# Kernel optimization log

Hardware: AMD Instinct MI355X
Metric: run time of the kernel (lower is better)

Reference implementation:

```python
import jax, jax.numpy as jnp
import numpy as np

NEG = float(-2**32 + 1)  # mask fill value used by the original module
H = 8  # number of heads (matches init kwarg h)


def setup_inputs() -> dict:
    key = jax.random.key(0)
    B, S, D, Q, V = 4, 2048, 512, 64, 64
    ks = jax.random.split(key, 10)
    sc = 1.0 / np.sqrt(D)
    x = jax.random.normal(ks[0], (B, S, D), jnp.float32)
    padding_mask = jax.random.randint(ks[1], (B, S), 0, 2, jnp.int32)
    Wq = jax.random.normal(ks[2], (H * Q, D), jnp.float32) * sc
    bq = jnp.zeros((H * Q,), jnp.float32)
    Wk = jax.random.normal(ks[3], (H * Q, D), jnp.float32) * sc
    bk = jnp.zeros((H * Q,), jnp.float32)
    Wv = jax.random.normal(ks[4], (H * V, D), jnp.float32) * sc
    bv = jnp.zeros((H * V,), jnp.float32)
    Wo = jax.random.normal(ks[5], (D, H * V), jnp.float32) * (1.0 / np.sqrt(H * V))
    bo = jnp.zeros((D,), jnp.float32)
    return {"x": x, "padding_mask": padding_mask, "Wq": Wq, "bq": bq,
            "Wk": Wk, "bk": bk, "Wv": Wv, "bv": bv, "Wo": Wo, "bo": bo}


def reference(x, padding_mask, Wq, bq, Wk, bk, Wv, bv, Wo, bo):
    # stage is hardcoded to 'train' (mask=True in init), so the causal branch runs.
    B, S, D = x.shape
    q_dim = Wq.shape[0] // H
    v_dim = Wv.shape[0] // H

    def split_heads(t, d):
        # torch: cat(chunk(h, dim=-1), dim=0) -> head-major [H*B, S, d]
        return t.reshape(B, S, H, d).transpose(2, 0, 1, 3).reshape(H * B, S, d)

    Qh = split_heads(x @ Wq.T + bq, q_dim)   # [H*B, S, q]
    Kh = split_heads(x @ Wk.T + bk, q_dim)
    Vh = split_heads(x @ Wv.T + bv, v_dim)

    score = jnp.einsum('nsd,ntd->nst', Qh, Kh) / jnp.sqrt(jnp.float32(q_dim))  # [H*B,S,S]
    pre_score = score  # module returns the UNMASKED scores (saved before masking)

    # causal mask (mask=True, stage=='train')
    causal = jnp.tril(jnp.ones((S, S), jnp.float32))
    score = jnp.where(causal > 0, score, NEG)

    # padding mask: built batch-major [B*H,S,S] while score is head-major [H*B,...]
    # -- faithful reproduction of the original ordering quirk.
    pm = jnp.broadcast_to(padding_mask[:, None, None, :], (B, H, S, S)).reshape(B * H, S, S)
    score = jnp.where(pm == 0, NEG, score)

    attn = jax.nn.softmax(score, axis=-1)
    out = jnp.einsum('nst,ntd->nsd', attn, Vh)  # [H*B, S, v]

    # torch: cat(chunk(h, dim=0), dim=-1) -> [B, S, H*v]
    heads = out.reshape(H, B, S, v_dim).transpose(1, 2, 0, 3).reshape(B, S, H * v_dim)
    self_attention = heads @ Wo.T + bo
    return self_attention, pre_score
```

## Files before the change

### kernel.cpp

```cpp
#include <hip/hip_runtime.h>
#include <hip/hip_fp16.h>
#include <math.h>

typedef _Float16 f16;
typedef _Float16 f16x8 __attribute__((ext_vector_type(8)));
typedef _Float16 f16x4 __attribute__((ext_vector_type(4)));
typedef float    f32x4 __attribute__((ext_vector_type(4)));

#define MFMA16(a,b,c) __builtin_amdgcn_mfma_f32_16x16x32_f16(a, b, c, 0, 0, 0)

#define MASKNEG (-6.0e9f)
#define LOG2E   1.44269504088896f

__global__ __launch_bounds__(256) void qkv_gemm(
    const float* __restrict__ x,
    const float* __restrict__ Wq, const float* __restrict__ bq,
    const float* __restrict__ Wk, const float* __restrict__ bk,
    const float* __restrict__ Wv, const float* __restrict__ bv,
    f16* __restrict__ Qws, f16* __restrict__ Kws, f16* __restrict__ Vt)
{
    __shared__ f16 Al[128 * 48];
    __shared__ f16 Wl[64 * 48];

    const int tid = threadIdx.x;
    const int bx  = blockIdx.x;
    const int m0  = blockIdx.y * 128;
    const int widx = bx >> 3;
    const int n0   = (bx & 7) * 64;

    const float* W    = (widx == 0) ? Wq : (widx == 1) ? Wk : Wv;
    const float* bias = (widx == 0) ? bq : (widx == 1) ? bk : bv;

    const int wid = tid >> 6, lane = tid & 63;
    const int g = lane >> 4, c = lane & 15;
    const int wm = (wid >> 1) * 64, wn = (wid & 1) * 32;

    const int sr = tid >> 3, sc = tid & 7;

    f32x4 acc[4][2] = {};

    for (int kk = 0; kk < 512; kk += 32) {
        __syncthreads();
        #pragma unroll
        for (int rr = 0; rr < 4; ++rr) {
            int row = sr + rr * 32;
            float4 v = *(const float4*)&x[(size_t)(m0 + row) * 512 + kk + sc * 4];
            f16x4 h4 = {(f16)v.x, (f16)v.y, (f16)v.z, (f16)v.w};
            *(f16x4*)&Al[row * 48 + sc * 4] = h4;
        }
        #pragma unroll
        for (int rr = 0; rr < 2; ++rr) {
            int row = sr + rr * 32;
            float4 v = *(const float4*)&W[(size_t)(n0 + row) * 512 + kk + sc * 4];
            f16x4 h4 = {(f16)v.x, (f16)v.y, (f16)v.z, (f16)v.w};
            *(f16x4*)&Wl[row * 48 + sc * 4] = h4;
        }
        __syncthreads();

        f16x8 b0 = *(const f16x8*)&Wl[(wn +  0 + c) * 48 + g * 8];
        f16x8 b1 = *(const f16x8*)&Wl[(wn + 16 + c) * 48 + g * 8];
        #pragma unroll
        for (int mf = 0; mf < 4; ++mf) {
            f16x8 a = *(const f16x8*)&Al[(wm + mf * 16 + c) * 48 + g * 8];
            acc[mf][0] = MFMA16(a, b0, acc[mf][0]);
            acc[mf][1] = MFMA16(a, b1, acc[mf][1]);
        }
    }

    #pragma unroll
    for (int nf = 0; nf < 2; ++nf) {
        int cc = n0 + wn + nf * 16 + c;
        float bval = bias[cc];
        #pragma unroll
        for (int mf = 0; mf < 4; ++mf) {
            if (widx < 2) {
                f16* outp = (widx == 0) ? Qws : Kws;
                #pragma unroll
                for (int r = 0; r < 4; ++r) {
                    int mrow = m0 + wm + mf * 16 + g * 4 + r;
                    outp[(size_t)mrow * 512 + cc] = (f16)(acc[mf][nf][r] + bval);
                }
            } else {
                int h  = n0 >> 6;
                int d  = wn + nf * 16 + c;
                int t0 = m0 + wm + mf * 16 + g * 4;
                int b  = t0 >> 11;
                int ts = t0 & 2047;
                int nn = h * 4 + b;
                f16x4 pk = {(f16)(acc[mf][nf][0] + bval), (f16)(acc[mf][nf][1] + bval),
                            (f16)(acc[mf][nf][2] + bval), (f16)(acc[mf][nf][3] + bval)};
                *(f16x4*)&Vt[((size_t)(nn * 64 + d)) * 2048 + ts] = pk;
            }
        }
    }
}

__global__ __launch_bounds__(256) void vsum_kernel(
    const f16* __restrict__ Vt, float* __restrict__ Vsum)
{
    const int row  = blockIdx.x * 4 + (threadIdx.x >> 6);
    const int lane = threadIdx.x & 63;
    const f16* p = Vt + (size_t)row * 2048;
    float s = 0.f;
    #pragma unroll
    for (int i = 0; i < 4; ++i) {
        f16x8 v = *(const f16x8*)&p[i * 512 + lane * 8];
        #pragma unroll
        for (int j = 0; j < 8; ++j) s += (float)v[j];
    }
    #pragma unroll
    for (int off = 1; off < 64; off <<= 1) s += __shfl_xor(s, off, 64);
    if (lane == 0) Vsum[row] = s;
}

__global__ __launch_bounds__(256) void attn_kernel(
    const f16* __restrict__ Qws, const f16* __restrict__ Kws,
    const f16* __restrict__ Vt,  const int* __restrict__ pmask,
    const float* __restrict__ Vsum,
    float* __restrict__ pre_score, f16* __restrict__ attn_out)
{
    __shared__ f16 Kl[64 * 72];
    __shared__ f16 Vl[64 * 72];
    __shared__ f16 Pl[4][32 * 72];

    const int tid = threadIdx.x;
    const int wid = tid >> 6, lane = tid & 63;
    const int g = lane >> 4, c = lane & 15;
    const int qt = blockIdx.x;
    const int n  = blockIdx.y;
    const int h = n >> 2, b = n & 3;
    const int pmrow = n >> 3;
    const int qlo = qt * 64 + wid * 16;
    const int qhi = (31 - qt) * 64 + wid * 16;

    f16x8 qf[2][2];
    #pragma unroll
    for (int ks = 0; ks < 2; ++ks) {
        qf[0][ks] = *(const f16x8*)
            &Qws[(size_t)(b * 2048 + qlo + c) * 512 + h * 64 + ks * 32 + g * 8];
        qf[1][ks] = *(const f16x8*)
            &Qws[(size_t)(b * 2048 + qhi + c) * 512 + h * 64 + ks * 32 + g * 8];
    }

    f32x4 o[2][4] = {};
    float mrow[2][4], lrow[2][4];
    #pragma unroll
    for (int mi = 0; mi < 2; ++mi)
        #pragma unroll
        for (int r = 0; r < 4; ++r) { mrow[mi][r] = -INFINITY; lrow[mi][r] = 0.0f; }

    const int sr = tid >> 3, sc = tid & 7;
    const int* pmp = pmask + pmrow * 2048;
    const f16* Kbase = Kws + (size_t)(b * 2048) * 512 + h * 64;
    const f16* Vbase = Vt + (size_t)(n * 64) * 2048;
    float* prow0 = pre_score + ((size_t)n * 2048 + qlo + g * 4) * 2048;
    float* prow1 = pre_score + ((size_t)n * 2048 + qhi + g * 4) * 2048;

    auto tile = [&](int kt, bool L0, bool L1) __attribute__((always_inline)) {
        __syncthreads();
        #pragma unroll
        for (int rr = 0; rr < 2; ++rr) {
            int row = sr + rr * 32;
            *(uint4*)&Kl[row * 72 + sc * 8] =
                *(const uint4*)&Kbase[(size_t)(kt * 64 + row) * 512 + sc * 8];
            *(uint4*)&Vl[row * 72 + sc * 8] =
                *(const uint4*)&Vbase[(size_t)row * 2048 + kt * 64 + sc * 8];
        }
        __syncthreads();

        f32x4 s[2][4] = {};
        #pragma unroll
        for (int nf = 0; nf < 4; ++nf)
            #pragma unroll
            for (int ks = 0; ks < 2; ++ks) {
                f16x8 kf = *(const f16x8*)&Kl[(nf * 16 + c) * 72 + ks * 32 + g * 8];
                s[0][nf] = MFMA16(qf[0][ks], kf, s[0][nf]);
                s[1][nf] = MFMA16(qf[1][ks], kf, s[1][nf]);
            }

        #pragma unroll
        for (int nf = 0; nf < 4; ++nf) {
            int tg  = kt * 64 + nf * 16 + c;
            int pmv = pmp[tg];
            #pragma unroll
            for (int r = 0; r < 4; ++r) {
                float v0 = s[0][nf][r] * 0.125f;
                float v1 = s[1][nf][r] * 0.125f;
                __builtin_nontemporal_store(v0, &prow0[(size_t)r * 2048 + tg]);
                __builtin_nontemporal_store(v1, &prow1[(size_t)r * 2048 + tg]);
                if (L0) s[0][nf][r] = (tg <= qlo + g * 4 + r && pmv != 0)
                                    ? v0 * LOG2E : MASKNEG;
                if (L1) s[1][nf][r] = (tg <= qhi + g * 4 + r && pmv != 0)
                                    ? v1 * LOG2E : MASKNEG;
            }
        }

        #pragma unroll
        for (int mi = 0; mi < 2; ++mi) {
            if (mi == 0 && !L0) continue;
            if (mi == 1 && !L1) continue;
            float alpha[4];
            #pragma unroll
            for (int r = 0; r < 4; ++r) {
                float rm = fmaxf(fmaxf(s[mi][0][r], s[mi][1][r]),
                                 fmaxf(s[mi][2][r], s[mi][3][r]));
                rm = fmaxf(rm, __shfl_xor(rm, 1, 64));
                rm = fmaxf(rm, __shfl_xor(rm, 2, 64));
                rm = fmaxf(rm, __shfl_xor(rm, 4, 64));
                rm = fmaxf(rm, __shfl_xor(rm, 8, 64));
                float mn = fmaxf(mrow[mi][r], rm);
                alpha[r] = exp2f(mrow[mi][r] - mn);
                mrow[mi][r] = mn;
            }
            float rs[4] = {0.f, 0.f, 0.f, 0.f};
            #pragma unroll
            for (int nf = 0; nf < 4; ++nf)
                #pragma unroll
                for (int r = 0; r < 4; ++r) {
                    float p = exp2f(s[mi][nf][r] - mrow[mi][r]);
                    rs[r] += p;
                    Pl[wid][(mi * 16 + g * 4 + r) * 72 + nf * 16 + c] = (f16)p;
                }
            #pragma unroll
            for (int r = 0; r < 4; ++r) {
                float t = rs[r];
                t += __shfl_xor(t, 1, 64);
                t += __shfl_xor(t, 2, 64);
                t += __shfl_xor(t, 4, 64);
                t += __shfl_xor(t, 8, 64);
                lrow[mi][r] = lrow[mi][r] * alpha[r] + t;
                #pragma unroll
                for (int dn = 0; dn < 4; ++dn) o[mi][dn][r] *= alpha[r];
            }
        }
        asm volatile("s_waitcnt lgkmcnt(0)" ::: "memory");

        #pragma unroll
        for (int ks = 0; ks < 2; ++ks) {
            f16x8 pa0, pa1;
            if (L0) pa0 = *(const f16x8*)&Pl[wid][( 0 + c) * 72 + ks * 32 + g * 8];
            if (L1) pa1 = *(const f16x8*)&Pl[wid][(16 + c) * 72 + ks * 32 + g * 8];
            #pragma unroll
            for (int dn = 0; dn < 4; ++dn) {
                f16x8 vb = *(const f16x8*)&Vl[(dn * 16 + c) * 72 + ks * 32 + g * 8];
                if (L0) o[0][dn] = MFMA16(pa0, vb, o[0][dn]);
                if (L1) o[1][dn] = MFMA16(pa1, vb, o[1][dn]);
            }
        }
    };

    for (int kt = 0; kt <= qt; ++kt)          tile(kt, true,  true);
    for (int kt = qt + 1; kt <= 31 - qt; ++kt) tile(kt, false, true);

    for (int kt = 32 - qt; kt < 32; ++kt) {
        f32x4 s[2][4] = {};
        #pragma unroll
        for (int nf = 0; nf < 4; ++nf)
            #pragma unroll
            for (int ks = 0; ks < 2; ++ks) {
                f16x8 kf = *(const f16x8*)
                    &Kbase[(size_t)(kt * 64 + nf * 16 + c) * 512 + ks * 32 + g * 8];
                s[0][nf] = MFMA16(qf[0][ks], kf, s[0][nf]);
                s[1][nf] = MFMA16(qf[1][ks], kf, s[1][nf]);
            }
        #pragma unroll
        for (int nf = 0; nf < 4; ++nf) {
            int tg = kt * 64 + nf * 16 + c;
            #pragma unroll
            for (int r = 0; r < 4; ++r) {
                __builtin_nontemporal_store(s[0][nf][r] * 0.125f,
                                            &prow0[(size_t)r * 2048 + tg]);
                __builtin_nontemporal_store(s[1][nf][r] * 0.125f,
                                            &prow1[(size_t)r * 2048 + tg]);
            }
        }
    }

    #pragma unroll
    for (int mi = 0; mi < 2; ++mi) {
        int qb = mi ? qhi : qlo;
        #pragma unroll
        for (int r = 0; r < 4; ++r) {
            int srow = qb + g * 4 + r;
            bool dead = (mrow[mi][r] == MASKNEG);
            float inv_l = dead ? 0.f : 1.0f / lrow[mi][r];
            #pragma unroll
            for (int dn = 0; dn < 4; ++dn) {
                float val = dead ? Vsum[n * 64 + dn * 16 + c] * (1.0f / 2048.0f)
                                 : o[mi][dn][r] * inv_l;
                attn_out[(size_t)(b * 2048 + srow) * 512 + h * 64 + dn * 16 + c] = (f16)val;
            }
        }
    }
}

__global__ __launch_bounds__(256) void out_gemm(
    const f16* __restrict__ Aattn, const float* __restrict__ Wo,
    const float* __restrict__ bo, float* __restrict__ outp)
{
    __shared__ f16 Al[128 * 48];
    __shared__ f16 Wl[64 * 48];

    const int tid = threadIdx.x;
    const int n0 = blockIdx.x * 64;
    const int m0 = blockIdx.y * 128;
    const int wid = tid >> 6, lane = tid & 63;
    const int g = lane >> 4, c = lane & 15;
    const int wm = (wid >> 1) * 64, wn = (wid & 1) * 32;

    const int sr4 = tid >> 2, sc4 = tid & 3;
    const int sr8 = tid >> 3, sc8 = tid & 7;

    f32x4 acc[4][2] = {};

    for (int kk = 0; kk < 512; kk += 32) {
        __syncthreads();
        #pragma unroll
        for (int rr = 0; rr < 2; ++rr) {
            int row = sr4 + rr * 64;
            *(uint4*)&Al[row * 48 + sc4 * 8] =
                *(const uint4*)&Aattn[(size_t)(m0 + row) * 512 + kk + sc4 * 8];
        }
        #pragma unroll
        for (int rr = 0; rr < 2; ++rr) {
            int row = sr8 + rr * 32;
            float4 v = *(const float4*)&Wo[(size_t)(n0 + row) * 512 + kk + sc8 * 4];
            f16x4 h4 = {(f16)v.x, (f16)v.y, (f16)v.z, (f16)v.w};
            *(f16x4*)&Wl[row * 48 + sc8 * 4] = h4;
        }
        __syncthreads();

        f16x8 b0 = *(const f16x8*)&Wl[(wn +  0 + c) * 48 + g * 8];
        f16x8 b1 = *(const f16x8*)&Wl[(wn + 16 + c) * 48 + g * 8];
        #pragma unroll
        for (int mf = 0; mf < 4; ++mf) {
            f16x8 a = *(const f16x8*)&Al[(wm + mf * 16 + c) * 48 + g * 8];
            acc[mf][0] = MFMA16(a, b0, acc[mf][0]);
            acc[mf][1] = MFMA16(a, b1, acc[mf][1]);
        }
    }

    #pragma unroll
    for (int nf = 0; nf < 2; ++nf) {
        int cc = n0 + wn + nf * 16 + c;
        float bval = bo[cc];
        #pragma unroll
        for (int mf = 0; mf < 4; ++mf)
            #pragma unroll
            for (int r = 0; r < 4; ++r)
                outp[(size_t)(m0 + wm + mf * 16 + g * 4 + r) * 512 + cc] =
                    acc[mf][nf][r] + bval;
    }
}

extern "C" void kernel_launch(void* const* d_in, const int* in_sizes, int n_in,
                              void* d_out, int out_size, void* d_ws, size_t ws_size,
                              hipStream_t stream)
{
    (void)in_sizes; (void)n_in; (void)out_size; (void)ws_size;

    const float* x  = (const float*)d_in[0];
    const int*   pm = (const int*)  d_in[1];
    const float* Wq = (const float*)d_in[2];
    const float* bq = (const float*)d_in[3];
    const float* Wk = (const float*)d_in[4];
    const float* bk = (const float*)d_in[5];
    const float* Wv = (const float*)d_in[6];
    const float* bv = (const float*)d_in[7];
    const float* Wo = (const float*)d_in[8];
    const float* bo = (const float*)d_in[9];

    float* out = (float*)d_out;
    float* pre = out + (size_t)4 * 2048 * 512;

    f16*   Qws  = (f16*)d_ws;
    f16*   Kws  = Qws + (size_t)8192 * 512;
    f16*   Vt   = Kws + (size_t)8192 * 512;
    f16*   Aat  = Vt  + (size_t)2048 * 2048;
    float* Vsum = (float*)(Aat + (size_t)8192 * 512);

    qkv_gemm   <<<dim3(24, 64), 256, 0, stream>>>(x, Wq, bq, Wk, bk, Wv, bv, Qws, Kws, Vt);
    vsum_kernel<<<dim3(512),    256, 0, stream>>>(Vt, Vsum);
    attn_kernel<<<dim3(16, 32), 256, 0, stream>>>(Qws, Kws, Vt, pm, Vsum, pre, Aat);
    out_gemm   <<<dim3(8, 64),  256, 0, stream>>>(Aat, Wo, bo, out);
}
```

Baseline: 308.4 us.

## Transpose QK MFMA, prefetch K/V into registers, precompute padding bias in LDS

Swaps the MFMA operand order so each lane holds four contiguous key columns of one query row. This lets pre_score be written as f32x4 vector stores instead of scattered scalar nontemporal stores, and makes row max/sum reductions need only two cross-lane shuffles. The 1/sqrt(d) scale is folded into the Q projection. The padding mask is turned into an additive bias table in shared memory, and the next tile's K/V global loads are issued into registers before the current tile's compute. The cost is shuffles to broadcast alpha and l back to the output layout, a threshold-based dead-row test, and 8 KB more LDS per block, which may reduce occupancy.

```diff
diff --git a/kernel.cpp b/kernel.cpp
--- a/kernel.cpp
+++ b/kernel.cpp
@@ -10,6 +10,7 @@
 #define MFMA16(a,b,c) __builtin_amdgcn_mfma_f32_16x16x32_f16(a, b, c, 0, 0, 0)
 
 #define MASKNEG (-6.0e9f)
+#define DEADTHR (-1.0e9f)
 #define LOG2E   1.44269504088896f
 
 __global__ __launch_bounds__(256) void qkv_gemm(
@@ -30,11 +31,11 @@
 
     const float* W    = (widx == 0) ? Wq : (widx == 1) ? Wk : Wv;
     const float* bias = (widx == 0) ? bq : (widx == 1) ? bk : bv;
+    const float scl  = (widx == 0) ? 0.125f : 1.0f;
 
     const int wid = tid >> 6, lane = tid & 63;
     const int g = lane >> 4, c = lane & 15;
     const int wm = (wid >> 1) * 64, wn = (wid & 1) * 32;
-
     const int sr = tid >> 3, sc = tid & 7;
 
     f32x4 acc[4][2] = {};
@@ -78,7 +79,7 @@
                 #pragma unroll
                 for (int r = 0; r < 4; ++r) {
                     int mrow = m0 + wm + mf * 16 + g * 4 + r;
-                    outp[(size_t)mrow * 512 + cc] = (f16)(acc[mf][nf][r] + bval);
+                    outp[(size_t)mrow * 512 + cc] = (f16)((acc[mf][nf][r] + bval) * scl);
                 }
             } else {
                 int h  = n0 >> 6;
@@ -122,6 +123,7 @@
     __shared__ f16 Kl[64 * 72];
     __shared__ f16 Vl[64 * 72];
     __shared__ f16 Pl[4][32 * 72];
+    __shared__ float Bias[2048];
 
     const int tid = threadIdx.x;
     const int wid = tid >> 6, lane = tid & 63;
@@ -132,6 +134,21 @@
     const int pmrow = n >> 3;
     const int qlo = qt * 64 + wid * 16;
     const int qhi = (31 - qt) * 64 + wid * 16;
+    const int qrel = wid * 16 + c;
+
+    {
+        const int i0 = tid * 8;
+        const int4* p4 = (const int4*)(pmask + pmrow * 2048 + i0);
+        int4 m0 = p4[0], m1 = p4[1];
+        Bias[i0 + 0] = m0.x ? 0.f : MASKNEG;
+        Bias[i0 + 1] = m0.y ? 0.f : MASKNEG;
+        Bias[i0 + 2] = m0.z ? 0.f : MASKNEG;
+        Bias[i0 + 3] = m0.w ? 0.f : MASKNEG;
+        Bias[i0 + 4] = m1.x ? 0.f : MASKNEG;
+        Bias[i0 + 5] = m1.y ? 0.f : MASKNEG;
+        Bias[i0 + 6] = m1.z ? 0.f : MASKNEG;
+        Bias[i0 + 7] = m1.w ? 0.f : MASKNEG;
+    }
 
     f16x8 qf[2][2];
     #pragma unroll
@@ -143,94 +160,105 @@
     }
 
     f32x4 o[2][4] = {};
-    float mrow[2][4], lrow[2][4];
-    #pragma unroll
-    for (int mi = 0; mi < 2; ++mi)
-        #pragma unroll
-        for (int r = 0; r < 4; ++r) { mrow[mi][r] = -INFINITY; lrow[mi][r] = 0.0f; }
+    float mrow[2] = {-INFINITY, -INFINITY};
+    float lrow[2] = {0.f, 0.f};
 
     const int sr = tid >> 3, sc = tid & 7;
-    const int* pmp = pmask + pmrow * 2048;
     const f16* Kbase = Kws + (size_t)(b * 2048) * 512 + h * 64;
     const f16* Vbase = Vt + (size_t)(n * 64) * 2048;
-    float* prow0 = pre_score + ((size_t)n * 2048 + qlo + g * 4) * 2048;
-    float* prow1 = pre_score + ((size_t)n * 2048 + qhi + g * 4) * 2048;
-
-    auto tile = [&](int kt, bool L0, bool L1) __attribute__((always_inline)) {
-        __syncthreads();
-        #pragma unroll
-        for (int rr = 0; rr < 2; ++rr) {
-            int row = sr + rr * 32;
-            *(uint4*)&Kl[row * 72 + sc * 8] =
-                *(const uint4*)&Kbase[(size_t)(kt * 64 + row) * 512 + sc * 8];
-            *(uint4*)&Vl[row * 72 + sc * 8] =
-                *(const uint4*)&Vbase[(size_t)row * 2048 + kt * 64 + sc * 8];
-        }
-        __syncthreads();
-
-        f32x4 s[2][4] = {};
-        #pragma unroll
-        for (int nf = 0; nf < 4; ++nf)
+    float* prow0 = pre_score + ((size_t)n * 2048 + qlo + c) * 2048;
+    float* prow1 = pre_score + ((size_t)n * 2048 + qhi + c) * 2048;
+
+    const int stageEnd = 32 - qt;
+
+    uint4 ka0, ka1, va0, va1;
+    auto glbload = [&](int kt) {
+        ka0 = *(const uint4*)&Kbase[(size_t)(kt * 64 + sr) * 512 + sc * 8];
+        ka1 = *(const uint4*)&Kbase[(size_t)(kt * 64 + sr + 32) * 512 + sc * 8];
+        va0 = *(const uint4*)&Vbase[(size_t)sr * 2048 + kt * 64 + sc * 8];
+        va1 = *(const uint4*)&Vbase[(size_t)(sr + 32) * 2048 + kt * 64 + sc * 8];
+    };
+
+    glbload(0);
+    for (int kt = 0; kt < stageEnd; ++kt) {
+        asm volatile("s_waitcnt lgkmcnt(0)" ::: "memory");
+        __builtin_amdgcn_s_barrier();
+        *(uint4*)&Kl[sr * 72 + sc * 8]        = ka0;
+        *(uint4*)&Kl[(sr + 32) * 72 + sc * 8] = ka1;
+        *(uint4*)&Vl[sr * 72 + sc * 8]        = va0;
+        *(uint4*)&Vl[(sr + 32) * 72 + sc * 8] = va1;
+        asm volatile("s_waitcnt lgkmcnt(0)" ::: "memory");
+        __builtin_amdgcn_s_barrier();
+        if (kt + 1 < stageEnd) glbload(kt + 1);
+
+        f32x4 s2[2][4] = {};
+        #pragma unroll
+        for (int kc = 0; kc < 4; ++kc)
             #pragma unroll
             for (int ks = 0; ks < 2; ++ks) {
-                f16x8 kf = *(const f16x8*)&Kl[(nf * 16 + c) * 72 + ks * 32 + g * 8];
-                s[0][nf] = MFMA16(qf[0][ks], kf, s[0][nf]);
-                s[1][nf] = MFMA16(qf[1][ks], kf, s[1][nf]);
-            }
-
-        #pragma unroll
-        for (int nf = 0; nf < 4; ++nf) {
-            int tg  = kt * 64 + nf * 16 + c;
-            int pmv = pmp[tg];
-            #pragma unroll
-            for (int r = 0; r < 4; ++r) {
-                float v0 = s[0][nf][r] * 0.125f;
-                float v1 = s[1][nf][r] * 0.125f;
-                __builtin_nontemporal_store(v0, &prow0[(size_t)r * 2048 + tg]);
-                __builtin_nontemporal_store(v1, &prow1[(size_t)r * 2048 + tg]);
-                if (L0) s[0][nf][r] = (tg <= qlo + g * 4 + r && pmv != 0)
-                                    ? v0 * LOG2E : MASKNEG;
-                if (L1) s[1][nf][r] = (tg <= qhi + g * 4 + r && pmv != 0)
-                                    ? v1 * LOG2E : MASKNEG;
-            }
-        }
+                f16x8 kf = *(const f16x8*)&Kl[(kc * 16 + c) * 72 + ks * 32 + g * 8];
+                s2[0][kc] = MFMA16(kf, qf[0][ks], s2[0][kc]);
+                s2[1][kc] = MFMA16(kf, qf[1][ks], s2[1][kc]);
+            }
+
+        #pragma unroll
+        for (int kc = 0; kc < 4; ++kc) {
+            *(f32x4*)&prow0[kt * 64 + kc * 16 + g * 4] = s2[0][kc];
+            *(f32x4*)&prow1[kt * 64 + kc * 16 + g * 4] = s2[1][kc];
+        }
+
+        f32x4 bi[4];
+        #pragma unroll
+        for (int kc = 0; kc < 4; ++kc)
+            bi[kc] = *(const f32x4*)&Bias[kt * 64 + kc * 16 + g * 4];
+
+        const bool L0 = (kt <= qt);
+        const bool bnd0 = (kt == qt), bnd1 = (kt == 31 - qt);
 
         #pragma unroll
         for (int mi = 0; mi < 2; ++mi) {
             if (mi == 0 && !L0) continue;
-            if (mi == 1 && !L1) continue;
-            float alpha[4];
-            #pragma unroll
-            for (int r = 0; r < 4; ++r) {
-                float rm = fmaxf(fmaxf(s[mi][0][r], s[mi][1][r]),
-                                 fmaxf(s[mi][2][r], s[mi][3][r]));
-                rm = fmaxf(rm, __shfl_xor(rm, 1, 64));
-                rm = fmaxf(rm, __shfl_xor(rm, 2, 64));
-                rm = fmaxf(rm, __shfl_xor(rm, 4, 64));
-                rm = fmaxf(rm, __shfl_xor(rm, 8, 64));
-                float mn = fmaxf(mrow[mi][r], rm);
-                alpha[r] = exp2f(mrow[mi][r] - mn);
-                mrow[mi][r] = mn;
-            }
-            float rs[4] = {0.f, 0.f, 0.f, 0.f};
-            #pragma unroll
-            for (int nf = 0; nf < 4; ++nf)
+            const bool bnd = mi ? bnd1 : bnd0;
+            float sl[4][4];
+            #pragma unroll
+            for (int kc = 0; kc < 4; ++kc)
                 #pragma unroll
                 for (int r = 0; r < 4; ++r) {
-                    float p = exp2f(s[mi][nf][r] - mrow[mi][r]);
-                    rs[r] += p;
-                    Pl[wid][(mi * 16 + g * 4 + r) * 72 + nf * 16 + c] = (f16)p;
+                    float sv = s2[mi][kc][r] + bi[kc][r];
+                    int klocal = kc * 16 + g * 4 + r;
+                    sl[kc][r] = (bnd && klocal > qrel) ? MASKNEG : sv;
                 }
+            float rm = sl[0][0];
+            #pragma unroll
+            for (int kc = 0; kc < 4; ++kc)
+                #pragma unroll
+                for (int r = 0; r < 4; ++r) rm = fmaxf(rm, sl[kc][r]);
+            rm = fmaxf(rm, __shfl_xor(rm, 16, 64));
+            rm = fmaxf(rm, __shfl_xor(rm, 32, 64));
+            float mn = fmaxf(mrow[mi], rm);
+            float alpha = exp2f((mrow[mi] - mn) * LOG2E);
+            mrow[mi] = mn;
+            float ml2 = mn * LOG2E;
+            float rs = 0.f;
+            #pragma unroll
+            for (int kc = 0; kc < 4; ++kc) {
+                f16x4 pk;
+                #pragma unroll
+                for (int r = 0; r < 4; ++r) {
+                    float p = exp2f(fmaf(sl[kc][r], LOG2E, -ml2));
+                    rs += p;
+                    pk[r] = (f16)p;
+                }
+                *(f16x4*)&Pl[wid][(mi * 16 + c) * 72 + kc * 16 + g * 4] = pk;
+            }
+            rs += __shfl_xor(rs, 16, 64);
+            rs += __shfl_xor(rs, 32, 64);
+            lrow[mi] = lrow[mi] * alpha + rs;
             #pragma unroll
             for (int r = 0; r < 4; ++r) {
-                float t = rs[r];
-                t += __shfl_xor(t, 1, 64);
-                t += __shfl_xor(t, 2, 64);
-                t += __shfl_xor(t, 4, 64);
-                t += __shfl_xor(t, 8, 64);
-                lrow[mi][r] = lrow[mi][r] * alpha[r] + t;
+                float af = __shfl(alpha, g * 4 + r, 64);
                 #pragma unroll
-                for (int dn = 0; dn < 4; ++dn) o[mi][dn][r] *= alpha[r];
+                for (int dn = 0; dn < 4; ++dn) o[mi][dn][r] *= af;
             }
         }
         asm volatile("s_waitcnt lgkmcnt(0)" ::: "memory");
@@ -239,40 +267,31 @@
         for (int ks = 0; ks < 2; ++ks) {
             f16x8 pa0, pa1;
             if (L0) pa0 = *(const f16x8*)&Pl[wid][( 0 + c) * 72 + ks * 32 + g * 8];
-            if (L1) pa1 = *(const f16x8*)&Pl[wid][(16 + c) * 72 + ks * 32 + g * 8];
+            pa1 = *(const f16x8*)&Pl[wid][(16 + c) * 72 + ks * 32 + g * 8];
             #pragma unroll
             for (int dn = 0; dn < 4; ++dn) {
                 f16x8 vb = *(const f16x8*)&Vl[(dn * 16 + c) * 72 + ks * 32 + g * 8];
                 if (L0) o[0][dn] = MFMA16(pa0, vb, o[0][dn]);
-                if (L1) o[1][dn] = MFMA16(pa1, vb, o[1][dn]);
-            }
-        }
-    };
-
-    for (int kt = 0; kt <= qt; ++kt)          tile(kt, true,  true);
-    for (int kt = qt + 1; kt <= 31 - qt; ++kt) tile(kt, false, true);
-
-    for (int kt = 32 - qt; kt < 32; ++kt) {
-        f32x4 s[2][4] = {};
-        #pragma unroll
-        for (int nf = 0; nf < 4; ++nf)
+                o[1][dn] = MFMA16(pa1, vb, o[1][dn]);
+            }
+        }
+    }
+
+    for (int kt = stageEnd; kt < 32; ++kt) {
+        f32x4 s2[2][4] = {};
+        #pragma unroll
+        for (int kc = 0; kc < 4; ++kc)
             #pragma unroll
             for (int ks = 0; ks < 2; ++ks) {
                 f16x8 kf = *(const f16x8*)
-                    &Kbase[(size_t)(kt * 64 + nf * 16 + c) * 512 + ks * 32 + g * 8];
-                s[0][nf] = MFMA16(qf[0][ks], kf, s[0][nf]);
-                s[1][nf] = MFMA16(qf[1][ks], kf, s[1][nf]);
-            }
-        #pragma unroll
-        for (int nf = 0; nf < 4; ++nf) {
-            int tg = kt * 64 + nf * 16 + c;
-            #pragma unroll
-            for (int r = 0; r < 4; ++r) {
-                __builtin_nontemporal_store(s[0][nf][r] * 0.125f,
-                                            &prow0[(size_t)r * 2048 + tg]);
-                __builtin_nontemporal_store(s[1][nf][r] * 0.125f,
-                                            &prow1[(size_t)r * 2048 + tg]);
-            }
+                    &Kbase[(size_t)(kt * 64 + kc * 16 + c) * 512 + ks * 32 + g * 8];
+                s2[0][kc] = MFMA16(kf, qf[0][ks], s2[0][kc]);
+                s2[1][kc] = MFMA16(kf, qf[1][ks], s2[1][kc]);
+            }
+        #pragma unroll
+        for (int kc = 0; kc < 4; ++kc) {
+            *(f32x4*)&prow0[kt * 64 + kc * 16 + g * 4] = s2[0][kc];
+            *(f32x4*)&prow1[kt * 64 + kc * 16 + g * 4] = s2[1][kc];
         }
     }
 
@@ -281,9 +300,11 @@
         int qb = mi ? qhi : qlo;
         #pragma unroll
         for (int r = 0; r < 4; ++r) {
+            float lo = __shfl(lrow[mi], g * 4 + r, 64);
+            float mo = __shfl(mrow[mi], g * 4 + r, 64);
             int srow = qb + g * 4 + r;
-            bool dead = (mrow[mi][r] == MASKNEG);
-            float inv_l = dead ? 0.f : 1.0f / lrow[mi][r];
+            bool dead = (mo < DEADTHR);
+            float inv_l = dead ? 0.f : 1.0f / lo;
             #pragma unroll
             for (int dn = 0; dn < 4; ++dn) {
                 float val = dead ? Vsum[n * 64 + dn * 16 + c] * (1.0f / 2048.0f)
```

Result: faster. 286.0 us (-7.3%).
